# Optimization experiments

Measured on AMD Instinct MI355X. Metric: run time of the kernel, lower is better.

The kernel has to match this reference:

```python
import jax, jax.numpy as jnp
import numpy as np

B, TQ, TK, F, H = 8, 2048, 2048, 1024, 1024


def setup_inputs() -> dict:
    key = jax.random.key(0)
    ks = jax.random.split(key, 9)
    scale = 1.0 / np.sqrt(F)
    query = jax.random.normal(ks[0], (B, TQ, F), dtype=jnp.float32)
    encoder_states = jax.random.normal(ks[1], (B, TK, F), dtype=jnp.float32)
    # boolean attention mask; True = keep. Random Bernoulli(0.5).
    target_mask = jax.random.randint(ks[2], (B, TQ, TK), 0, 2) > 0
    # Linear params (torch nn.Linear: y = x @ W.T + b); store W as [F, H] for x @ W.
    Wq = jax.random.normal(ks[3], (F, H), dtype=jnp.float32) * scale
    bq = jax.random.normal(ks[4], (H,), dtype=jnp.float32) * scale
    Wk = jax.random.normal(ks[5], (F, H), dtype=jnp.float32) * scale
    bk = jax.random.normal(ks[6], (H,), dtype=jnp.float32) * scale
    Wv = jax.random.normal(ks[7], (F, H), dtype=jnp.float32) * scale
    bv = jax.random.normal(ks[8], (H,), dtype=jnp.float32) * scale
    return {"query": query, "encoder_states": encoder_states, "target_mask": target_mask,
            "Wq": Wq, "bq": bq, "Wk": Wk, "bk": bk, "Wv": Wv, "bv": bv}


def reference(query, encoder_states, target_mask, Wq, bq, Wk, bk, Wv, bv):
    # init(): K/V projections of encoder states
    K = jnp.einsum('btf,fh->bth', encoder_states, Wk) + bk   # [B,TK,H]
    V = jnp.einsum('btf,fh->bth', encoder_states, Wv) + bv   # [B,TK,H]
    # forward()
    Q = jnp.einsum('btf,fh->bth', query, Wq) + bq            # [B,TQ,H]
    scores = jnp.einsum('bqh,bkh->bqk', Q, K) / jnp.sqrt(jnp.asarray(H, Q.dtype))
    scores = jnp.where(target_mask, scores, -jnp.inf)
    attn = jax.nn.softmax(scores, axis=-1)                   # [B,TQ,TK]
    return jnp.einsum('bqk,bkh->bqh', attn, V)               # [B,TQ,H]
```

## Files before the change

### kernel.cpp

```cpp
#include <hip/hip_runtime.h>

#define NB 8
#define TQv 2048
#define TKv 2048
#define FD 1024
#define HD 1024

typedef __attribute__((ext_vector_type(8))) short short8;
typedef __attribute__((ext_vector_type(8))) _Float16 half8;
typedef __attribute__((ext_vector_type(4))) float f32x4;

__device__ __forceinline__ short f2bf(float f) {
    union { float f; unsigned u; } v; v.f = f;
    unsigned r = v.u + 0x7FFFu + ((v.u >> 16) & 1u);
    return (short)(r >> 16);
}

__device__ __forceinline__ half8 as_h8(short8 v) {
    union { short8 s; half8 h; } u; u.s = v; return u.h;
}

__device__ __forceinline__ void async16(const short* g, short* l) {
    __builtin_amdgcn_global_load_lds(
        (const __attribute__((address_space(1))) unsigned int*)g,
        (__attribute__((address_space(3))) unsigned int*)l, 16, 0, 0);
}

__device__ __forceinline__ unsigned lds_off(void* p) {
    return (unsigned)(unsigned long long)(__attribute__((address_space(3))) char*)p;
}

#define BAR  __builtin_amdgcn_s_barrier()
#define SP1  __builtin_amdgcn_s_setprio(1)
#define SP0  __builtin_amdgcn_s_setprio(0)
#define SCB  __builtin_amdgcn_sched_barrier(0)
#define VMCNT(N) asm volatile("s_waitcnt vmcnt(" #N ")" ::: "memory")
#define LGKC(N)  asm volatile("s_waitcnt lgkmcnt(" #N ")" ::: "memory")

#define DSR(dst, addr, OFS) \
    asm volatile("ds_read_b128 %0, %1 offset:" OFS : "=v"(dst) : "v"(addr))

#define RD_ALO(BF) { DSR(aQ0[0][0], adA0[BF], "0");    DSR(aQ0[0][1], adA1[BF], "0"); \
                     DSR(aQ0[1][0], adA0[BF], "2048"); DSR(aQ0[1][1], adA1[BF], "2048"); \
                     DSR(aQ0[2][0], adA0[BF], "4096"); DSR(aQ0[2][1], adA1[BF], "4096"); \
                     DSR(aQ0[3][0], adA0[BF], "6144"); DSR(aQ0[3][1], adA1[BF], "6144"); }
#define RD_AHI(BF) { DSR(aQ1[0][0], adA0[BF], "8192");  DSR(aQ1[0][1], adA1[BF], "8192"); \
                     DSR(aQ1[1][0], adA0[BF], "10240"); DSR(aQ1[1][1], adA1[BF], "10240"); \
                     DSR(aQ1[2][0], adA0[BF], "12288"); DSR(aQ1[2][1], adA1[BF], "12288"); \
                     DSR(aQ1[3][0], adA0[BF], "14336"); DSR(aQ1[3][1], adA1[BF], "14336"); }
#define RD_BLO(BF) { DSR(bQ0[0][0], adB0[BF], "0");    DSR(bQ0[0][1], adB1[BF], "0"); \
                     DSR(bQ0[1][0], adB0[BF], "2048"); DSR(bQ0[1][1], adB1[BF], "2048"); }
#define RD_BHI(BF) { DSR(bQ1[0][0], adB0[BF], "4096"); DSR(bQ1[0][1], adB1[BF], "4096"); \
                     DSR(bQ1[1][0], adB0[BF], "6144"); DSR(bQ1[1][1], adB1[BF], "6144"); }

#define QMFMA(AQ, BQ, MO, NO) { \
    _Pragma("unroll") for (int ks = 0; ks < 2; ++ks) \
    _Pragma("unroll") for (int f = 0; f < 4; ++f) \
    _Pragma("unroll") for (int n = 0; n < 2; ++n) { \
        if constexpr (F16) \
            acc[(MO)+f][(NO)+n] = __builtin_amdgcn_mfma_f32_16x16x32_f16( \
                as_h8(AQ[f][ks]), as_h8(BQ[n][ks]), acc[(MO)+f][(NO)+n], 0, 0, 0); \
        else \
            acc[(MO)+f][(NO)+n] = __builtin_amdgcn_mfma_f32_16x16x32_bf16( \
                AQ[f][ks], BQ[n][ks], acc[(MO)+f][(NO)+n], 0, 0, 0); } }

#define STG_A(BF, H, REL) { \
    async16(gaBase + sH[2*(H)+0] + tofs + (REL), lbase + (BF)*32768 + (H)*8192); \
    async16(gaBase + sH[2*(H)+1] + tofs + (REL), lbase + (BF)*32768 + (H)*8192 + 4096); }
#define STG_B(BF, H, REL) { \
    async16(gbBase + sH[2*(H)+0] + tofs + (REL), lbase + (BF)*32768 + 16384 + (H)*8192); \
    async16(gbBase + sH[2*(H)+1] + tofs + (REL), lbase + (BF)*32768 + 16384 + (H)*8192 + 4096); }

template <bool F16>
__device__ __forceinline__ void gemm256_core(const short* __restrict__ A,
                                             const short* __restrict__ B,
                                             int ld, int K, char* smem,
                                             f32x4 acc[8][4], int tid) {
    const int wid = tid >> 6, lane = tid & 63;
    const int wm = wid >> 2, wn = wid & 3;
    const int l15 = lane & 15;

    const int kc8 = ((lane & 7) ^ (lane >> 3)) * 8;
    const short* gaBase = A + (size_t)(wid * 8 + (lane >> 3)) * ld + kc8;
    const short* gbBase = B + (size_t)(wid * 8 + (lane >> 3)) * ld + kc8;
    size_t sH[4];
#pragma unroll
    for (int k = 0; k < 4; ++k) sH[k] = (size_t)k * 64 * ld;
    short* lbase = (short*)smem + wid * 512;

    const int o0 = (((lane >> 4)    ) ^ (lane & 7)) * 16;
    const int o1 = (((lane >> 4) + 4) ^ (lane & 7)) * 16;
    unsigned aB_ = lds_off(smem) + wm * 16384 + l15 * 128;
    unsigned bB_ = lds_off(smem) + 32768 + (wn >> 1) * 16384 + (wn & 1) * 8192 + l15 * 128;
    unsigned adA0[2] = { aB_ + o0, aB_ + o0 + 65536u };
    unsigned adA1[2] = { aB_ + o1, aB_ + o1 + 65536u };
    unsigned adB0[2] = { bB_ + o0, bB_ + o0 + 65536u };
    unsigned adB1[2] = { bB_ + o1, bB_ + o1 + 65536u };

    int tofs = 0;
    STG_A(0, 0, 0); STG_A(0, 1, 0); STG_B(0, 0, 0); STG_B(0, 1, 0);
    STG_A(1, 0, 64); STG_A(1, 1, 64);
    SCB; VMCNT(4); BAR; SCB;

    short8 aQ0[4][2], aQ1[4][2], bQ0[2][2], bQ1[2][2];
    const int niter = K >> 7;
    for (int it = 0; it < niter; ++it) {
        const bool nl = (it != niter - 1);
        RD_ALO(0); RD_BLO(0);
        STG_B(1, 0, 64);
        SCB; LGKC(8); BAR; LGKC(0); SCB;
        SP1; QMFMA(aQ0, bQ0, 0, 0); SP0; SCB; BAR; SCB;
        RD_AHI(0);
        STG_B(1, 1, 64);
        SCB; BAR; LGKC(0); SCB;
        SP1; QMFMA(aQ1, bQ0, 4, 0); SP0; SCB; BAR; SCB;
        RD_BHI(0);
        if (nl) STG_A(0, 0, 128);
        SCB; BAR; LGKC(0); SCB;
        SP1; QMFMA(aQ0, bQ1, 0, 2); SP0; SCB; BAR; SCB;
        if (nl) { STG_A(0, 1, 128); SCB; VMCNT(4); } else { SCB; VMCNT(0); }
        BAR;
        SP1; QMFMA(aQ1, bQ1, 4, 2); SP0; SCB; BAR; SCB;
        RD_ALO(1); RD_BLO(1);
        if (nl) STG_B(0, 0, 128);
        SCB; LGKC(8); BAR; LGKC(0); SCB;
        SP1; QMFMA(aQ0, bQ0, 0, 0); SP0; SCB; BAR; SCB;
        RD_AHI(1);
        if (nl) STG_B(0, 1, 128);
        SCB; BAR; LGKC(0); SCB;
        SP1; QMFMA(aQ1, bQ0, 4, 0); SP0; SCB; BAR; SCB;
        RD_BHI(1);
        if (nl) STG_A(1, 0, 192);
        SCB; BAR; LGKC(0); SCB;
        SP1; QMFMA(aQ0, bQ1, 0, 2); SP0; SCB; BAR; SCB;
        if (nl) { STG_A(1, 1, 192); SCB; VMCNT(4); }
        BAR;
        SP1; QMFMA(aQ1, bQ1, 4, 2); SP0; SCB; BAR; SCB;
        tofs += 128;
    }
}


__global__ __launch_bounds__(256) void convert_kernel(const float* __restrict__ q,
                                                      const float* __restrict__ e,
                                                      short* __restrict__ xq,
                                                      short* __restrict__ xe) {
    size_t i = (size_t)blockIdx.x * 256 + threadIdx.x;
    const float* src = blockIdx.y ? e : q;
    short* dst = blockIdx.y ? xe : xq;
    float4 a = ((const float4*)src)[2 * i];
    float4 b = ((const float4*)src)[2 * i + 1];
    short8 v;
    v[0] = f2bf(a.x); v[1] = f2bf(a.y); v[2] = f2bf(a.z); v[3] = f2bf(a.w);
    v[4] = f2bf(b.x); v[5] = f2bf(b.y); v[6] = f2bf(b.z); v[7] = f2bf(b.w);
    ((short8*)dst)[i] = v;
}

__global__ __launch_bounds__(256) void wtrans_kernel(const float* __restrict__ Wq,
                                                     const float* __restrict__ Wk,
                                                     const float* __restrict__ Wv,
                                                     short* __restrict__ Wt) {
    __shared__ float tile[32][33];
    const float* W = (blockIdx.z == 0) ? Wq : (blockIdx.z == 1) ? Wk : Wv;
    short* dst = Wt + (size_t)blockIdx.z * HD * FD;
    int h0 = blockIdx.x * 32, f0 = blockIdx.y * 32;
    int tx = threadIdx.x, ty = threadIdx.y;
    for (int j = ty; j < 32; j += 8)
        tile[j][tx] = W[(size_t)(f0 + j) * HD + h0 + tx];
    __syncthreads();
    for (int j = ty; j < 32; j += 8)
        dst[(size_t)(h0 + j) * FD + f0 + tx] = f2bf(tile[tx][j]);
}

__global__ __launch_bounds__(512, 2) void projqk_kernel(const short* __restrict__ Xq,
                                                        const short* __restrict__ Xe,
                                                        const short* __restrict__ Wt3,
                                                        const float* __restrict__ bq,
                                                        const float* __restrict__ bk,
                                                        short* __restrict__ Q,
                                                        short* __restrict__ K) {
    extern __shared__ char smem[];
    int tid = threadIdx.x;
    int p = blockIdx.z;
    const short* X = p ? Xe : Xq;
    const short* Wt = Wt3 + (size_t)p * HD * FD;
    const float* bias = p ? bk : bq;
    short* O = p ? K : Q;
    int bid = blockIdx.x;
    int xcd = bid & 7, idx = bid >> 3;
    int n_t = idx & 3, m_t = (idx >> 2) * 8 + xcd;
    int tile_m = m_t * 256, tile_n = n_t * 256;
    f32x4 acc[8][4] = {};
    gemm256_core<false>(X + (size_t)tile_m * FD, Wt + (size_t)tile_n * FD, FD, FD, smem, acc, tid);
    int wid = tid >> 6, lane = tid & 63;
    int wm = wid >> 2, wn = wid & 3;
    int row0 = tile_m + wm * 128 + ((lane >> 4) << 2);
    int col0 = tile_n + wn * 64 + (lane & 15);
#pragma unroll
    for (int n = 0; n < 4; ++n) {
        int gn = col0 + n * 16;
        float bv_ = bias[gn];
#pragma unroll
        for (int m = 0; m < 8; ++m)
#pragma unroll
            for (int r = 0; r < 4; ++r)
                O[(size_t)(row0 + m * 16 + r) * HD + gn] = f2bf(acc[m][n][r] + bv_);
    }
}

__global__ __launch_bounds__(512, 2) void projv_kernel(const short* __restrict__ Xe,
                                                       const short* __restrict__ Wtv,
                                                       const float* __restrict__ bv,
                                                       short* __restrict__ Vt) {
    extern __shared__ char smem[];
    int tid = threadIdx.x;
    int bid = blockIdx.x;
    int b = bid & 7, i = bid >> 3;
    int m_t = i & 3, n_t = i >> 2;
    int tile_m = m_t * 256, tile_n = n_t * 256;
    const short* Xb = Xe + (size_t)b * TKv * FD;
    f32x4 acc[8][4] = {};
    gemm256_core<false>(Wtv + (size_t)tile_m * FD, Xb + (size_t)tile_n * FD, FD, FD, smem, acc, tid);
    short* Ob = Vt + (size_t)b * HD * TKv;
    int wid = tid >> 6, lane = tid & 63;
    int wm = wid >> 2, wn = wid & 3;
    int row0 = tile_m + wm * 128 + ((lane >> 4) << 2);
    int col0 = tile_n + wn * 64 + (lane & 15);
#pragma unroll
    for (int m = 0; m < 8; ++m)
#pragma unroll
        for (int r = 0; r < 4; ++r) {
            int gm = row0 + m * 16 + r;
            float bv_ = bv[gm];
#pragma unroll
            for (int n = 0; n < 4; ++n) {
                union { _Float16 h; short s; } cv;
                cv.h = (_Float16)(acc[m][n][r] + bv_);
                Ob[(size_t)gm * TKv + col0 + n * 16] = cv.s;
            }
        }
}

__global__ __launch_bounds__(256) void maskbits_kernel(const int* __restrict__ mask,
                                                       unsigned long long* __restrict__ Mbits,
                                                       float* __restrict__ L) {
    int tid = threadIdx.x;
    int lane = tid & 63;
    if (blockIdx.x < 64) L[blockIdx.x * 256 + tid] = 0.f;
    const int NW = NB * TQv * (TKv / 64);
    int stride = gridDim.x * 4;
    for (int w = blockIdx.x * 4 + (tid >> 6); w < NW; w += stride) {
        int v = mask[(size_t)w * 64 + lane];
        unsigned long long bal = __ballot(v != 0);
        if (lane == 0) Mbits[w] = bal;
    }
}

__global__ __launch_bounds__(512, 2) void score_kernel(const short* __restrict__ Q,
                                                       const short* __restrict__ K,
                                                       const unsigned long long* __restrict__ Mbits,
                                                       short* __restrict__ S,
                                                       float* __restrict__ L) {
    extern __shared__ char smem[];
    int tid = threadIdx.x;
    int bid = blockIdx.x;
    int b = bid & 7, i = bid >> 3;
    int n_t = i & 7, m_t = i >> 3;
    int tile_m = m_t * 256, tile_n = n_t * 256;
    const short* Aq = Q + (size_t)b * TQv * HD;
    const short* Bk = K + (size_t)b * TKv * HD;
    f32x4 acc[8][4] = {};
    gemm256_core<false>(Aq + (size_t)tile_m * HD, Bk + (size_t)tile_n * HD, HD, HD, smem, acc, tid);
    short* Sb = S + (size_t)b * TQv * TKv;
    float* Lb = L + (size_t)b * TQv;
    int wid = tid >> 6, lane = tid & 63;
    int wm = wid >> 2, wn = wid & 3;
    int l15 = lane & 15;
    int row0 = tile_m + wm * 128 + ((lane >> 4) << 2);
    int col0 = tile_n + wn * 64 + l15;

    {
        const unsigned long long* MbT = Mbits + (size_t)b * TQv * (TKv / 64)
                                        + (size_t)tile_m * (TKv / 64) + (tile_n >> 6);
        async16((const short*)(MbT + (size_t)(tid >> 1) * (TKv / 64) + (size_t)(tid & 1) * 2),
                (short*)smem + wid * 512);
    }
    __syncthreads();

#pragma unroll
    for (int m = 0; m < 8; ++m)
#pragma unroll
        for (int r = 0; r < 4; ++r) {
            int rl = wm * 128 + m * 16 + ((lane >> 4) << 2) + r;
            int gm = tile_m + rl;
            unsigned long long bits = *(const unsigned long long*)(smem + rl * 32 + wn * 8);
            float rs = 0.f;
#pragma unroll
            for (int n = 0; n < 4; ++n) {
                float pv = ((bits >> (n * 16 + l15)) & 1ULL)
                               ? exp2f(acc[m][n][r] * 0.04508422f - 5.77078016f) : 0.f;
                rs += pv;
                union { _Float16 h; short sh; } cv;
                cv.h = (_Float16)pv;
                Sb[(size_t)gm * TKv + col0 + n * 16] = cv.sh;
            }
            for (int sh = 1; sh < 16; sh <<= 1) rs += __shfl_xor(rs, sh);
            if (l15 == 0) atomicAdd(&Lb[gm], rs);
        }
}

__global__ __launch_bounds__(512, 2) void pv_kernel(const short* __restrict__ P,
                                                    const short* __restrict__ Vt,
                                                    const float* __restrict__ L,
                                                    float* __restrict__ Out) {
    extern __shared__ char smem[];
    int tid = threadIdx.x;
    int bid = blockIdx.x;
    int b = bid & 7, i = bid >> 3;
    int n_t = i & 3, m_t = i >> 2;
    int tile_m = m_t * 256, tile_n = n_t * 256;
    const short* Ap = P + (size_t)b * TQv * TKv;
    const short* Bv = Vt + (size_t)b * HD * TKv;
    const float* Lb = L + (size_t)b * TQv;
    f32x4 acc[8][4] = {};
    gemm256_core<true>(Ap + (size_t)tile_m * TKv, Bv + (size_t)tile_n * TKv, TKv, TKv, smem, acc, tid);
    float* Ob = Out + (size_t)b * TQv * HD;
    int wid = tid >> 6, lane = tid & 63;
    int wm = wid >> 2, wn = wid & 3;
    int row0 = tile_m + wm * 128 + ((lane >> 4) << 2);
    int col0 = tile_n + wn * 64 + (lane & 15);

    if (tid < 64)
        async16((const short*)(Lb + tile_m + tid * 4), (short*)smem);
    __syncthreads();

#pragma unroll
    for (int m = 0; m < 8; ++m)
#pragma unroll
        for (int r = 0; r < 4; ++r) {
            int rl = wm * 128 + m * 16 + ((lane >> 4) << 2) + r;
            int gm = tile_m + rl;
            float l = *(const float*)(smem + rl * 4);
            float inv = (l > 0.f) ? 1.f / l : 0.f;
#pragma unroll
            for (int n = 0; n < 4; ++n)
                Ob[(size_t)gm * HD + col0 + n * 16] = acc[m][n][r] * inv;
        }
}

extern "C" void kernel_launch(void* const* d_in, const int* in_sizes, int n_in,
                              void* d_out, int out_size, void* d_ws, size_t ws_size,
                              hipStream_t stream) {
    const float* query = (const float*)d_in[0];
    const float* enc   = (const float*)d_in[1];
    const int*   mask  = (const int*)d_in[2];
    const float* Wq    = (const float*)d_in[3];
    const float* bq    = (const float*)d_in[4];
    const float* Wk    = (const float*)d_in[5];
    const float* bk    = (const float*)d_in[6];
    const float* Wv    = (const float*)d_in[7];
    const float* bv    = (const float*)d_in[8];
    float* out = (float*)d_out;

    char* ws = (char*)d_ws;
    short* Wt  = (short*)(ws);
    unsigned long long* Mbits = (unsigned long long*)(ws);
    float* L   = (float*)(ws + 4194304);
    short* Xq  = (short*)(ws + 6291456);
    short* Xe  = (short*)(ws + 39845888);
    short* S   = (short*)(ws + 6291456);
    short* Qb  = (short*)(ws + 73400320);
    short* Kb  = (short*)(ws + 106954752);
    short* Vt  = (short*)(ws + 140509184);
    (void)in_sizes; (void)n_in; (void)out_size; (void)ws_size;

    static bool inited = false;
    if (!inited) {
        hipFuncSetAttribute((const void*)projqk_kernel, hipFuncAttributeMaxDynamicSharedMemorySize, 131072);
        hipFuncSetAttribute((const void*)projv_kernel,  hipFuncAttributeMaxDynamicSharedMemorySize, 131072);
        hipFuncSetAttribute((const void*)score_kernel,  hipFuncAttributeMaxDynamicSharedMemorySize, 131072);
        hipFuncSetAttribute((const void*)pv_kernel,     hipFuncAttributeMaxDynamicSharedMemorySize, 131072);
        inited = true;
    }

    convert_kernel<<<dim3(8192, 2), 256, 0, stream>>>(query, enc, Xq, Xe);
    wtrans_kernel<<<dim3(32, 32, 3), dim3(32, 8), 0, stream>>>(Wq, Wk, Wv, Wt);
    projqk_kernel<<<dim3(256, 1, 2), 512, 131072, stream>>>(Xq, Xe, Wt, bq, bk, Qb, Kb);
    projv_kernel<<<dim3(256), 512, 131072, stream>>>(Xe, Wt + (size_t)2 * HD * FD, bv, Vt);
    maskbits_kernel<<<dim3(2048), 256, 0, stream>>>(mask, Mbits, L);
    score_kernel<<<dim3(512), 512, 131072, stream>>>(Qb, Kb, Mbits, S, L);
    pv_kernel<<<dim3(256), 512, 131072, stream>>>(S, Vt, L, out);
}
```

Before: 578.4 us.

## Merge prep kernels into one launch and tighten GEMM mainloop barriers

Combines the fp32->bf16 convert, weight transpose and mask bit-packing kernels into a single prep_kernel dispatched by block index, removing two launches and letting the independent preprocessing work overlap. The GEMM mainloop now issues both A stage loads together and runs two MFMA groups back-to-back, dropping one barrier pair per half-iteration. The projection epilogue is reordered so the stores go row by row with the bias hoisted. The workspace is rearranged so Wt no longer aliases Mbits, at the cost of extra workspace, and the GEMM change raises register and VMEM pressure.

```diff
diff --git a/kernel.cpp b/kernel.cpp
--- a/kernel.cpp
+++ b/kernel.cpp
@@ -115,12 +115,11 @@
         SCB; BAR; LGKC(0); SCB;
         SP1; QMFMA(aQ1, bQ0, 4, 0); SP0; SCB; BAR; SCB;
         RD_BHI(0);
-        if (nl) STG_A(0, 0, 128);
+        if (nl) { STG_A(0, 0, 128); STG_A(0, 1, 128); }
         SCB; BAR; LGKC(0); SCB;
-        SP1; QMFMA(aQ0, bQ1, 0, 2); SP0; SCB; BAR; SCB;
-        if (nl) { STG_A(0, 1, 128); SCB; VMCNT(4); } else { SCB; VMCNT(0); }
-        BAR;
-        SP1; QMFMA(aQ1, bQ1, 4, 2); SP0; SCB; BAR; SCB;
+        SP1; QMFMA(aQ0, bQ1, 0, 2); QMFMA(aQ1, bQ1, 4, 2); SP0; SCB;
+        if (nl) { VMCNT(4); } else { VMCNT(0); }
+        BAR; SCB;
         RD_ALO(1); RD_BLO(1);
         if (nl) STG_B(0, 0, 128);
         SCB; LGKC(8); BAR; LGKC(0); SCB;
@@ -130,46 +129,66 @@
         SCB; BAR; LGKC(0); SCB;
         SP1; QMFMA(aQ1, bQ0, 4, 0); SP0; SCB; BAR; SCB;
         RD_BHI(1);
-        if (nl) STG_A(1, 0, 192);
+        if (nl) { STG_A(1, 0, 192); STG_A(1, 1, 192); }
         SCB; BAR; LGKC(0); SCB;
-        SP1; QMFMA(aQ0, bQ1, 0, 2); SP0; SCB; BAR; SCB;
-        if (nl) { STG_A(1, 1, 192); SCB; VMCNT(4); }
-        BAR;
-        SP1; QMFMA(aQ1, bQ1, 4, 2); SP0; SCB; BAR; SCB;
+        SP1; QMFMA(aQ0, bQ1, 0, 2); QMFMA(aQ1, bQ1, 4, 2); SP0; SCB;
+        if (nl) VMCNT(4);
+        BAR; SCB;
         tofs += 128;
     }
 }
 
 
-__global__ __launch_bounds__(256) void convert_kernel(const float* __restrict__ q,
-                                                      const float* __restrict__ e,
-                                                      short* __restrict__ xq,
-                                                      short* __restrict__ xe) {
-    size_t i = (size_t)blockIdx.x * 256 + threadIdx.x;
-    const float* src = blockIdx.y ? e : q;
-    short* dst = blockIdx.y ? xe : xq;
-    float4 a = ((const float4*)src)[2 * i];
-    float4 b = ((const float4*)src)[2 * i + 1];
-    short8 v;
-    v[0] = f2bf(a.x); v[1] = f2bf(a.y); v[2] = f2bf(a.z); v[3] = f2bf(a.w);
-    v[4] = f2bf(b.x); v[5] = f2bf(b.y); v[6] = f2bf(b.z); v[7] = f2bf(b.w);
-    ((short8*)dst)[i] = v;
-}
-
-__global__ __launch_bounds__(256) void wtrans_kernel(const float* __restrict__ Wq,
-                                                     const float* __restrict__ Wk,
-                                                     const float* __restrict__ Wv,
-                                                     short* __restrict__ Wt) {
+#define CONV_BLKS 16384
+#define WT_BLKS   3072
+#define MB_START  (CONV_BLKS + WT_BLKS)
+__global__ __launch_bounds__(256) void prep_kernel(const float* __restrict__ q,
+                                                   const float* __restrict__ e,
+                                                   const float* __restrict__ Wq,
+                                                   const float* __restrict__ Wk,
+                                                   const float* __restrict__ Wv,
+                                                   const int* __restrict__ mask,
+                                                   short* __restrict__ xq,
+                                                   short* __restrict__ xe,
+                                                   short* __restrict__ Wt,
+                                                   unsigned long long* __restrict__ Mbits,
+                                                   float* __restrict__ L) {
     __shared__ float tile[32][33];
-    const float* W = (blockIdx.z == 0) ? Wq : (blockIdx.z == 1) ? Wk : Wv;
-    short* dst = Wt + (size_t)blockIdx.z * HD * FD;
-    int h0 = blockIdx.x * 32, f0 = blockIdx.y * 32;
-    int tx = threadIdx.x, ty = threadIdx.y;
-    for (int j = ty; j < 32; j += 8)
-        tile[j][tx] = W[(size_t)(f0 + j) * HD + h0 + tx];
-    __syncthreads();
-    for (int j = ty; j < 32; j += 8)
-        dst[(size_t)(h0 + j) * FD + f0 + tx] = f2bf(tile[tx][j]);
+    int bid = blockIdx.x, tid = threadIdx.x;
+    if (bid < CONV_BLKS) {
+        size_t i = (size_t)(bid & 8191) * 256 + tid;
+        const float* src = (bid >> 13) ? e : q;
+        short* dst = (bid >> 13) ? xe : xq;
+        float4 a = ((const float4*)src)[2 * i];
+        float4 b = ((const float4*)src)[2 * i + 1];
+        short8 v;
+        v[0] = f2bf(a.x); v[1] = f2bf(a.y); v[2] = f2bf(a.z); v[3] = f2bf(a.w);
+        v[4] = f2bf(b.x); v[5] = f2bf(b.y); v[6] = f2bf(b.z); v[7] = f2bf(b.w);
+        ((short8*)dst)[i] = v;
+    } else if (bid < MB_START) {
+        int t = bid - CONV_BLKS;
+        int z = t >> 10, r2 = t & 1023;
+        const float* W = (z == 0) ? Wq : (z == 1) ? Wk : Wv;
+        short* dst = Wt + (size_t)z * HD * FD;
+        int h0 = (r2 & 31) * 32, f0 = (r2 >> 5) * 32;
+        int tx = tid & 31, ty = tid >> 5;
+        for (int j = ty; j < 32; j += 8)
+            tile[j][tx] = W[(size_t)(f0 + j) * HD + h0 + tx];
+        __syncthreads();
+        for (int j = ty; j < 32; j += 8)
+            dst[(size_t)(h0 + j) * FD + f0 + tx] = f2bf(tile[tx][j]);
+    } else {
+        int mb = bid - MB_START;
+        int lane = tid & 63;
+        if (mb < 64) L[mb * 256 + tid] = 0.f;
+        const int NW = NB * TQv * (TKv / 64);
+        int stride = 2048 * 4;
+        for (int w = mb * 4 + (tid >> 6); w < NW; w += stride) {
+            int v = mask[(size_t)w * 64 + lane];
+            unsigned long long bal = __ballot(v != 0);
+            if (lane == 0) Mbits[w] = bal;
+        }
+    }
 }
 
 __global__ __launch_bounds__(512, 2) void projqk_kernel(const short* __restrict__ Xq,
@@ -196,16 +215,18 @@
     int wm = wid >> 2, wn = wid & 3;
     int row0 = tile_m + wm * 128 + ((lane >> 4) << 2);
     int col0 = tile_n + wn * 64 + (lane & 15);
-#pragma unroll
-    for (int n = 0; n < 4; ++n) {
-        int gn = col0 + n * 16;
-        float bv_ = bias[gn];
-#pragma unroll
-        for (int m = 0; m < 8; ++m)
-#pragma unroll
-            for (int r = 0; r < 4; ++r)
-                O[(size_t)(row0 + m * 16 + r) * HD + gn] = f2bf(acc[m][n][r] + bv_);
-    }
+    float bv4[4];
+#pragma unroll
+    for (int n = 0; n < 4; ++n) bv4[n] = bias[col0 + n * 16];
+#pragma unroll
+    for (int m = 0; m < 8; ++m)
+#pragma unroll
+        for (int r = 0; r < 4; ++r) {
+            size_t rowb = (size_t)(row0 + m * 16 + r) * HD;
+#pragma unroll
+            for (int n = 0; n < 4; ++n)
+                O[rowb + col0 + n * 16] = f2bf(acc[m][n][r] + bv4[n]);
+        }
 }
 
 __global__ __launch_bounds__(512, 2) void projv_kernel(const short* __restrict__ Xe,
@@ -239,21 +260,6 @@
                 Ob[(size_t)gm * TKv + col0 + n * 16] = cv.s;
             }
         }
-}
-
-__global__ __launch_bounds__(256) void maskbits_kernel(const int* __restrict__ mask,
-                                                       unsigned long long* __restrict__ Mbits,
-                                                       float* __restrict__ L) {
-    int tid = threadIdx.x;
-    int lane = tid & 63;
-    if (blockIdx.x < 64) L[blockIdx.x * 256 + tid] = 0.f;
-    const int NW = NB * TQv * (TKv / 64);
-    int stride = gridDim.x * 4;
-    for (int w = blockIdx.x * 4 + (tid >> 6); w < NW; w += stride) {
-        int v = mask[(size_t)w * 64 + lane];
-        unsigned long long bal = __ballot(v != 0);
-        if (lane == 0) Mbits[w] = bal;
-    }
 }
 
 __global__ __launch_bounds__(512, 2) void score_kernel(const short* __restrict__ Q,
@@ -363,15 +369,15 @@
     float* out = (float*)d_out;
 
     char* ws = (char*)d_ws;
-    short* Wt  = (short*)(ws);
     unsigned long long* Mbits = (unsigned long long*)(ws);
     float* L   = (float*)(ws + 4194304);
-    short* Xq  = (short*)(ws + 6291456);
-    short* Xe  = (short*)(ws + 39845888);
-    short* S   = (short*)(ws + 6291456);
-    short* Qb  = (short*)(ws + 73400320);
-    short* Kb  = (short*)(ws + 106954752);
-    short* Vt  = (short*)(ws + 140509184);
+    short* Wt  = (short*)(ws + 4259840);
+    short* Xq  = (short*)(ws + 10551296);
+    short* Xe  = (short*)(ws + 44105728);
+    short* S   = (short*)(ws + 10551296);
+    short* Qb  = (short*)(ws + 77660160);
+    short* Kb  = (short*)(ws + 111214592);
+    short* Vt  = (short*)(ws + 144769024);
     (void)in_sizes; (void)n_in; (void)out_size; (void)ws_size;
 
     static bool inited = false;
@@ -383,11 +389,10 @@
         inited = true;
     }
 
-    convert_kernel<<<dim3(8192, 2), 256, 0, stream>>>(query, enc, Xq, Xe);
-    wtrans_kernel<<<dim3(32, 32, 3), dim3(32, 8), 0, stream>>>(Wq, Wk, Wv, Wt);
+    prep_kernel<<<dim3(CONV_BLKS + WT_BLKS + 2048), 256, 0, stream>>>(
+        query, enc, Wq, Wk, Wv, mask, Xq, Xe, Wt, Mbits, L);
     projqk_kernel<<<dim3(256, 1, 2), 512, 131072, stream>>>(Xq, Xe, Wt, bq, bk, Qb, Kb);
     projv_kernel<<<dim3(256), 512, 131072, stream>>>(Xe, Wt + (size_t)2 * HD * FD, bv, Vt);
-    maskbits_kernel<<<dim3(2048), 256, 0, stream>>>(mask, Mbits, L);
     score_kernel<<<dim3(512), 512, 131072, stream>>>(Qb, Kb, Mbits, S, L);
     pv_kernel<<<dim3(256), 512, 131072, stream>>>(S, Vt, L, out);
 }
```

After: 562.4 us. 2.8% less time.
